# Optimization experiments

Measured on AMD Instinct MI355X. Metric: run time of the kernel, lower is better.

Reference implementation:

```python
import jax, jax.numpy as jnp
import numpy as np
import math

KSIZE = 2.0
SIGMA = 3.0
EPS = 1e-05


def setup_inputs() -> dict:
    key = jax.random.key(0)
    kx, ky, kz = jax.random.split(key, 3)
    N, D = 8192, 64
    X = jax.random.normal(kx, (N, D), dtype=jnp.float32)
    Y = jax.random.normal(ky, (N, D), dtype=jnp.float32)
    Z = jax.random.normal(kz, (N, D), dtype=jnp.float32)
    return {"X": X, "Y": Y, "Z": Z}


def _mean_kernel(A, B, ksize):
    # mean over N x N RBF Gram: exp(-||a-b||^2 / ksize) / sqrt(2*pi*ksize)
    # squared distances via expansion (same math as sum((a-b)**2, -1))
    sq = (jnp.sum(A * A, axis=-1)[:, None]
          + jnp.sum(B * B, axis=-1)[None, :]
          - 2.0 * A @ B.T)
    norm = math.sqrt(2.0 * math.pi * ksize)
    return jnp.mean(jnp.exp(-sq / ksize)) / norm


def reference(X, Y, Z):
    ks = KSIZE
    mxx = _mean_kernel(X, X, ks)
    mzz = _mean_kernel(Z, Z, ks)
    mxz = _mean_kernel(X, Z, ks)
    mxy = _mean_kernel(X, Y, ks)
    myy = _mean_kernel(Y, Y, ks)
    myz = _mean_kernel(Y, Z, ks)
    r1 = jnp.log(SIGMA * jnp.sqrt(mxx * mzz + EPS) / (mxz + EPS))
    r2 = jnp.log(SIGMA * jnp.sqrt(myy * mzz + EPS) / (myz + EPS))
    r3 = jnp.log(SIGMA * jnp.sqrt(mxx * myy + EPS) / (mxy + EPS))
    return r1 * 10.0 + r2 + r3 * 10.0
```

## Files before the change

### kernel.cpp

```cpp
#include <hip/hip_runtime.h>
#include <math.h>

#define N 8192
#define D 64

typedef short bf16x8 __attribute__((ext_vector_type(8)));
typedef float f32x4 __attribute__((ext_vector_type(4)));

__device__ __forceinline__ void gload_lds16(const void* g, void* l) {
    __builtin_amdgcn_global_load_lds(
        (const __attribute__((address_space(1))) void*)g,
        (__attribute__((address_space(3))) void*)l, 16, 0, 0);
}

__global__ void init_accs(float* accs) {
    if (threadIdx.x < 6) accs[threadIdx.x] = 0.0f;
}

__global__ __launch_bounds__(256) void convert_norm(
        const float* __restrict__ X, const float* __restrict__ Y,
        const float* __restrict__ Z,
        unsigned short* __restrict__ bmat, float* __restrict__ nscl) {
    int wid  = blockIdx.x * 4 + (threadIdx.x >> 6);
    int lane = threadIdx.x & 63;
    int mat  = wid >> 13;
    int row  = wid & 8191;
    const float* src = (mat == 0) ? X : (mat == 1 ? Y : Z);
    float v = src[row * D + lane] * 1.2011224087864498f;
    unsigned int bits = __builtin_bit_cast(unsigned int, v);
    unsigned short us = (unsigned short)((bits + 0x7FFFu + ((bits >> 16) & 1u)) >> 16);
    float f = __builtin_bit_cast(float, (unsigned int)us << 16);
    bmat[(size_t)mat * (N * D) + row * D + lane] = us;
    float sq = f * f;
    #pragma unroll
    for (int off = 32; off; off >>= 1) sq += __shfl_xor(sq, off);
    if (lane == 0) nscl[mat * N + row] = sq * 0.5f;
}

__global__ __launch_bounds__(256, 6) void gram_kernel(
        const unsigned short* __restrict__ bmat,
        const float* __restrict__ nscl,
        float* __restrict__ accs) {
    const int PA[6] = {0, 2, 0, 0, 1, 1};
    const int PB[6] = {0, 2, 2, 1, 1, 2};
    int p  = blockIdx.y;
    int bx = blockIdx.x;
    int ti = bx >> 1;
    int tc = bx & 1;

    const unsigned short* A = bmat + (size_t)PA[p] * (N * D);
    const unsigned short* B = bmat + (size_t)PB[p] * (N * D);
    const float* ca = nscl + PA[p] * N;
    const float* cb = nscl + PB[p] * N;

    int tid = threadIdx.x;
    int w = tid >> 6, lane = tid & 63;
    int wr = w >> 1, wc = w & 1;
    int rowBase = ti * 64 + wr * 32;
    int r = lane & 15, q = lane >> 4, r7 = lane & 7;

    __shared__ __align__(128) char lds[3 * 8192];
    __shared__ float wsum[4];

    int sub = w * 2048;
    int laneoff = ((lane >> 3) << 7) + ((r7 ^ (lane >> 3)) << 4);
    const char* gB = (const char*)(B + (size_t)(tc * 4096) * D);

    int off0 = wc * 4096 + r * 128 + ((q ^ r7) << 4);
    int off1 = wc * 4096 + r * 128 + (((4 + q) ^ r7) << 4);

    {
        const char* g0 = gB + sub + laneoff;
        gload_lds16(g0,        lds + sub);
        gload_lds16(g0 + 1024, lds + sub + 1024);
        const char* g1 = gB + 8192 + sub + laneoff;
        gload_lds16(g1,        lds + 8192 + sub);
        gload_lds16(g1 + 1024, lds + 8192 + sub + 1024);
    }

    bf16x8 afrag[2][2];
    #pragma unroll
    for (int mt = 0; mt < 2; ++mt)
        #pragma unroll
        for (int kc = 0; kc < 2; ++kc)
            afrag[mt][kc] = *reinterpret_cast<const bf16x8*>(
                A + (size_t)(rowBase + mt * 16 + r) * D + kc * 32 + q * 8);
    f32x4 ncam[2];
    #pragma unroll
    for (int mt = 0; mt < 2; ++mt)
        #pragma unroll
        for (int e = 0; e < 4; ++e)
            ncam[mt][e] = -ca[rowBase + mt * 16 + q * 4 + e];

    const float* cbp = cb + tc * 4096 + wc * 32 + r;

    f32x4 lsum = (f32x4)0.0f;
    f32x4 acc0[2][2], acc1[2][2], acc2[2][2];

    #define EPI(ACC)                                                          \
    {                                                                         \
        float e0 = fmaxf(fmaxf(ACC[0][0][0], ACC[0][0][1]), ACC[0][0][2]);    \
        float e1 = fmaxf(fmaxf(ACC[0][0][3], ACC[0][1][0]), ACC[0][1][1]);    \
        float e2 = fmaxf(fmaxf(ACC[0][1][2], ACC[0][1][3]), ACC[1][0][0]);    \
        float e3 = fmaxf(fmaxf(ACC[1][0][1], ACC[1][0][2]), ACC[1][0][3]);    \
        float e4 = fmaxf(fmaxf(ACC[1][1][0], ACC[1][1][1]), ACC[1][1][2]);    \
        float e5 = fmaxf(fmaxf(e0, e1), e2);                                  \
        float e6 = fmaxf(fmaxf(e3, e4), ACC[1][1][3]);                        \
        float em = fmaxf(e5, e6);                                             \
        if (__any(em > -30.0f)) {                                             \
            _Pragma("unroll")                                                 \
            for (int mt = 0; mt < 2; ++mt) {                                  \
                _Pragma("unroll")                                             \
                for (int nt = 0; nt < 2; ++nt) {                              \
                    f32x4 ex;                                                 \
                    _Pragma("unroll")                                         \
                    for (int e = 0; e < 4; ++e)                               \
                        ex[e] = __builtin_amdgcn_exp2f(ACC[mt][nt][e]);       \
                    lsum += ex;                                               \
                }                                                             \
            }                                                                 \
        }                                                                     \
    }

    #define GSTEP(RB, SB, ACC, DO_EPI, ACCP, TT)                              \
    {                                                                         \
        asm volatile("s_waitcnt vmcnt(2)" ::: "memory");                      \
        __builtin_amdgcn_s_barrier();                                         \
        asm volatile("" ::: "memory");                                        \
        float cb0 = cbp[0], cb1 = cbp[16];                                    \
        int tn = ((TT) + 2 <= 63) ? ((TT) + 2) : 63;                          \
        const char* gs = gB + (size_t)tn * 8192 + sub + laneoff;              \
        gload_lds16(gs,        lds + (SB) + sub);                             \
        gload_lds16(gs + 1024, lds + (SB) + sub + 1024);                      \
        bf16x8 bf00 = *reinterpret_cast<const bf16x8*>(lds + (RB) + off0);    \
        bf16x8 bf01 = *reinterpret_cast<const bf16x8*>(lds + (RB) + off1);    \
        bf16x8 bf10 = *reinterpret_cast<const bf16x8*>(lds + (RB) + 2048 + off0); \
        bf16x8 bf11 = *reinterpret_cast<const bf16x8*>(lds + (RB) + 2048 + off1); \
        if (DO_EPI) EPI(ACCP);                                                \
        ACC[0][0] = ncam[0] - cb0; ACC[0][1] = ncam[0] - cb1;                 \
        ACC[1][0] = ncam[1] - cb0; ACC[1][1] = ncam[1] - cb1;                 \
        ACC[0][0] = __builtin_amdgcn_mfma_f32_16x16x32_bf16(afrag[0][0], bf00, ACC[0][0], 0, 0, 0); \
        ACC[0][1] = __builtin_amdgcn_mfma_f32_16x16x32_bf16(afrag[0][0], bf10, ACC[0][1], 0, 0, 0); \
        ACC[1][0] = __builtin_amdgcn_mfma_f32_16x16x32_bf16(afrag[1][0], bf00, ACC[1][0], 0, 0, 0); \
        ACC[1][1] = __builtin_amdgcn_mfma_f32_16x16x32_bf16(afrag[1][0], bf10, ACC[1][1], 0, 0, 0); \
        ACC[0][0] = __builtin_amdgcn_mfma_f32_16x16x32_bf16(afrag[0][1], bf01, ACC[0][0], 0, 0, 0); \
        ACC[0][1] = __builtin_amdgcn_mfma_f32_16x16x32_bf16(afrag[0][1], bf11, ACC[0][1], 0, 0, 0); \
        ACC[1][0] = __builtin_amdgcn_mfma_f32_16x16x32_bf16(afrag[1][1], bf01, ACC[1][0], 0, 0, 0); \
        ACC[1][1] = __builtin_amdgcn_mfma_f32_16x16x32_bf16(afrag[1][1], bf11, ACC[1][1], 0, 0, 0); \
        cbp += 64;                                                            \
    }

    GSTEP(0, 16384, acc0, false, acc0, 0)
    for (int trip = 0; trip < 21; ++trip) {
        int t1 = 1 + trip * 3;
        GSTEP(8192,  0,     acc1, true, acc0, t1)
        GSTEP(16384, 8192,  acc2, true, acc1, t1 + 1)
        GSTEP(0,     16384, acc0, true, acc2, t1 + 2)
    }
    EPI(acc0)

    #undef GSTEP
    #undef EPI

    float ls = lsum[0] + lsum[1] + lsum[2] + lsum[3];
    #pragma unroll
    for (int off = 32; off; off >>= 1) ls += __shfl_xor(ls, off);
    if (lane == 0) wsum[w] = ls;
    __syncthreads();
    if (tid == 0)
        atomicAdd(&accs[p], wsum[0] + wsum[1] + wsum[2] + wsum[3]);
}

__global__ void finalize_kernel(const float* __restrict__ accs,
                                float* __restrict__ out) {
    double inv = 1.0 / (8192.0 * 8192.0 * 3.5449077018110318);
    double mxx = accs[0] * inv, mzz = accs[1] * inv, mxz = accs[2] * inv;
    double mxy = accs[3] * inv, myy = accs[4] * inv, myz = accs[5] * inv;
    double r1 = log(3.0 * sqrt(mxx * mzz + 1e-5) / (mxz + 1e-5));
    double r2 = log(3.0 * sqrt(myy * mzz + 1e-5) / (myz + 1e-5));
    double r3 = log(3.0 * sqrt(mxx * myy + 1e-5) / (mxy + 1e-5));
    out[0] = (float)(10.0 * r1 + r2 + 10.0 * r3);
}

extern "C" void kernel_launch(void* const* d_in, const int* in_sizes, int n_in,
                              void* d_out, int out_size, void* d_ws, size_t ws_size,
                              hipStream_t stream) {
    const float* X = (const float*)d_in[0];
    const float* Y = (const float*)d_in[1];
    const float* Z = (const float*)d_in[2];
    char* ws = (char*)d_ws;
    unsigned short* bmat = (unsigned short*)ws;
    float* nscl = (float*)(ws + (size_t)3 * N * D * 2);
    float* accs = (float*)(ws + (size_t)3 * N * D * 2 + (size_t)3 * N * 4);
    float* out = (float*)d_out;

    hipLaunchKernelGGL(init_accs, dim3(1), dim3(64), 0, stream, accs);
    hipLaunchKernelGGL(convert_norm, dim3(3 * N / 4), dim3(256), 0, stream,
                       X, Y, Z, bmat, nscl);
    hipLaunchKernelGGL(gram_kernel, dim3(256, 6), dim3(256), 0, stream,
                       bmat, nscl, accs);
    hipLaunchKernelGGL(finalize_kernel, dim3(1), dim3(1), 0, stream, accs, out);
}
```

Baseline: 79.48 us.

## Double block to 512 threads so each B tile serves 128 A rows

Doubles the thread block to eight waves covering 128 A rows per block while keeping the 64-column B tile, so each staged B tile in LDS is reused across twice as many rows. Each wave now issues a single 16-byte async load per stage, and the vmcnt wait counts are adjusted to match. This halves global B traffic and the number of blocks and atomics. The cost is fewer blocks (768) for the GPU and larger barrier groups, which may hurt latency hiding and occupancy.

```diff
diff --git a/kernel.cpp b/kernel.cpp
--- a/kernel.cpp
+++ b/kernel.cpp
@@ -37,7 +37,7 @@
     if (lane == 0) nscl[mat * N + row] = sq * 0.5f;
 }
 
-__global__ __launch_bounds__(256, 6) void gram_kernel(
+__global__ __launch_bounds__(512, 6) void gram_kernel(
         const unsigned short* __restrict__ bmat,
         const float* __restrict__ nscl,
         float* __restrict__ accs) {
@@ -56,13 +56,13 @@
     int tid = threadIdx.x;
     int w = tid >> 6, lane = tid & 63;
     int wr = w >> 1, wc = w & 1;
-    int rowBase = ti * 64 + wr * 32;
+    int rowBase = ti * 128 + wr * 32;
     int r = lane & 15, q = lane >> 4, r7 = lane & 7;
 
     __shared__ __align__(128) char lds[3 * 8192];
-    __shared__ float wsum[4];
-
-    int sub = w * 2048;
+    __shared__ float wsum[8];
+
+    int sub = w * 1024;
     int laneoff = ((lane >> 3) << 7) + ((r7 ^ (lane >> 3)) << 4);
     const char* gB = (const char*)(B + (size_t)(tc * 4096) * D);
 
@@ -70,12 +70,8 @@
     int off1 = wc * 4096 + r * 128 + (((4 + q) ^ r7) << 4);
 
     {
-        const char* g0 = gB + sub + laneoff;
-        gload_lds16(g0,        lds + sub);
-        gload_lds16(g0 + 1024, lds + sub + 1024);
-        const char* g1 = gB + 8192 + sub + laneoff;
-        gload_lds16(g1,        lds + 8192 + sub);
-        gload_lds16(g1 + 1024, lds + 8192 + sub + 1024);
+        gload_lds16(gB + sub + laneoff,        lds + sub);
+        gload_lds16(gB + 8192 + sub + laneoff, lds + 8192 + sub);
     }
 
     bf16x8 afrag[2][2];
@@ -122,16 +118,14 @@
         }                                                                     \
     }
 
-    #define GSTEP(RB, SB, ACC, DO_EPI, ACCP, TT)                              \
+    #define GSTEP(RB, SB, ACC, DO_EPI, ACCP, TT, WAITN)                       \
     {                                                                         \
-        asm volatile("s_waitcnt vmcnt(2)" ::: "memory");                      \
+        asm volatile("s_waitcnt vmcnt(" #WAITN ")" ::: "memory");             \
         __builtin_amdgcn_s_barrier();                                         \
         asm volatile("" ::: "memory");                                        \
         float cb0 = cbp[0], cb1 = cbp[16];                                    \
         int tn = ((TT) + 2 <= 63) ? ((TT) + 2) : 63;                          \
-        const char* gs = gB + (size_t)tn * 8192 + sub + laneoff;              \
-        gload_lds16(gs,        lds + (SB) + sub);                             \
-        gload_lds16(gs + 1024, lds + (SB) + sub + 1024);                      \
+        gload_lds16(gB + (size_t)tn * 8192 + sub + laneoff, lds + (SB) + sub);\
         bf16x8 bf00 = *reinterpret_cast<const bf16x8*>(lds + (RB) + off0);    \
         bf16x8 bf01 = *reinterpret_cast<const bf16x8*>(lds + (RB) + off1);    \
         bf16x8 bf10 = *reinterpret_cast<const bf16x8*>(lds + (RB) + 2048 + off0); \
@@ -150,12 +144,12 @@
         cbp += 64;                                                            \
     }
 
-    GSTEP(0, 16384, acc0, false, acc0, 0)
+    GSTEP(0, 16384, acc0, false, acc0, 0, 1)
     for (int trip = 0; trip < 21; ++trip) {
         int t1 = 1 + trip * 3;
-        GSTEP(8192,  0,     acc1, true, acc0, t1)
-        GSTEP(16384, 8192,  acc2, true, acc1, t1 + 1)
-        GSTEP(0,     16384, acc0, true, acc2, t1 + 2)
+        GSTEP(8192,  0,     acc1, true, acc0, t1,     3)
+        GSTEP(16384, 8192,  acc2, true, acc1, t1 + 1, 3)
+        GSTEP(0,     16384, acc0, true, acc2, t1 + 2, 3)
     }
     EPI(acc0)
 
@@ -167,8 +161,12 @@
     for (int off = 32; off; off >>= 1) ls += __shfl_xor(ls, off);
     if (lane == 0) wsum[w] = ls;
     __syncthreads();
-    if (tid == 0)
-        atomicAdd(&accs[p], wsum[0] + wsum[1] + wsum[2] + wsum[3]);
+    if (tid == 0) {
+        float s = 0.0f;
+        #pragma unroll
+        for (int i = 0; i < 8; ++i) s += wsum[i];
+        atomicAdd(&accs[p], s);
+    }
 }
 
 __global__ void finalize_kernel(const float* __restrict__ accs,
@@ -197,7 +195,7 @@
     hipLaunchKernelGGL(init_accs, dim3(1), dim3(64), 0, stream, accs);
     hipLaunchKernelGGL(convert_norm, dim3(3 * N / 4), dim3(256), 0, stream,
                        X, Y, Z, bmat, nscl);
-    hipLaunchKernelGGL(gram_kernel, dim3(256, 6), dim3(256), 0, stream,
+    hipLaunchKernelGGL(gram_kernel, dim3(128, 6), dim3(512), 0, stream,
                        bmat, nscl, accs);
     hipLaunchKernelGGL(finalize_kernel, dim3(1), dim3(1), 0, stream, accs, out);
 }
```

Result: faster. 68.32 us (-14.0%).
